# Performance work log

Measured on AMD Instinct MI355X. Metric: run time of the kernel, lower is better.

## Reference

```python
import jax, jax.numpy as jnp
import numpy as np

N = 50000   # nodes
E = 800000  # edges (avg degree 16)
D = 128     # in_feats == out_feats


def setup_inputs() -> dict:
    key = jax.random.key(0)
    k1, k2, k3, k4 = jax.random.split(key, 4)
    h = jax.random.normal(k1, (N, D), dtype=jnp.float32)
    src = jax.random.randint(k2, (E,), 0, N, dtype=jnp.int32)
    dst = jax.random.randint(k3, (E,), 0, N, dtype=jnp.int32)
    snorm_n = jnp.ones((N, 1), dtype=jnp.float32)  # sqrt(1/N) replicated; identity-scaled here
    # NodeApply linear: Linear(2*D, D) with bias
    W = jax.random.normal(k4, (D, 2 * D), dtype=jnp.float32) / np.sqrt(2 * D).astype(np.float32)
    b = jnp.zeros((D,), dtype=jnp.float32)
    return {"h": h, "snorm_n": snorm_n, "W": W, "b": b, "src": src, "dst": dst}


def reference(h, snorm_n, W, b, src, dst):
    # dropout p=0.0 -> identity
    h_in = h
    # gather neighbor messages and segment-mean aggregate (MeanAggregator)
    ones = jnp.ones((src.shape[0],), dtype=h.dtype)
    deg = jax.ops.segment_sum(ones, dst, num_segments=N)            # [N]
    msg_sum = jax.ops.segment_sum(h[src], dst, num_segments=N)     # [N, D]
    c = msg_sum / jnp.maximum(deg, 1.0)[:, None]                   # zero-degree nodes -> c = 0
    # NodeApply: concat -> linear -> L2 normalize -> relu
    bundle = jnp.concatenate([h, c], axis=1) @ W.T + b             # [N, D]
    nrm = jnp.sqrt(jnp.sum(bundle * bundle, axis=1, keepdims=True))
    bundle = bundle / jnp.maximum(nrm, 1e-12)                      # F.normalize(p=2, dim=1)
    out = jax.nn.relu(bundle)
    # graph norm
    out = out * snorm_n
    # residual (in_feats == out_feats)
    return h_in + out
```

## Files before the change

kernel.cpp:

```cpp
#include <hip/hip_runtime.h>
#include <hip/hip_bf16.h>

#define TPB 256
#define CHUNK_LOG 13
#define CHUNK (1 << CHUNK_LOG)
#define HSTRIDE 12544

typedef __attribute__((ext_vector_type(8))) short bf16x8;
typedef __attribute__((ext_vector_type(4))) float f32x4;

__device__ inline unsigned short f2bf(float f) {
    unsigned u = __float_as_uint(f);
    unsigned r = u + 0x7fffu + ((u >> 16) & 1u);
    return (unsigned short)(r >> 16);
}
__device__ inline float bf2f(unsigned short s) {
    return __uint_as_float(((unsigned)s) << 16);
}
__device__ inline float lo16(unsigned u) { return __uint_as_float(u << 16); }
__device__ inline float hi16(unsigned u) { return __uint_as_float(u & 0xffff0000u); }

__global__ void k_conv(const float* __restrict__ h, const float* __restrict__ W,
                       unsigned short* __restrict__ h_hi,
                       unsigned short* __restrict__ Wb, int N) {
    int t = blockIdx.x * TPB + threadIdx.x;
    int nh4 = N * 32;
    if (t < nh4) {
        float4 v = ((const float4*)h)[t];
        ushort4 hi;
        hi.x = f2bf(v.x); hi.y = f2bf(v.y);
        hi.z = f2bf(v.z); hi.w = f2bf(v.w);
        ((ushort4*)h_hi)[t] = hi;
    } else if (t - nh4 < 8192) {
        int w4 = t - nh4;
        float4 v = ((const float4*)W)[w4];
        ushort4 hi;
        hi.x = f2bf(v.x); hi.y = f2bf(v.y);
        hi.z = f2bf(v.z); hi.w = f2bf(v.w);
        ((ushort4*)Wb)[w4] = hi;
    }
}

__global__ void k_hist(const int* __restrict__ dst,
                       unsigned* __restrict__ hist32, unsigned char* __restrict__ lrank,
                       int E) {
    __shared__ unsigned lhist[HSTRIDE];
    int b = blockIdx.x;
    for (int i = threadIdx.x; i < HSTRIDE; i += TPB) lhist[i] = 0;
    __syncthreads();
    int e0 = b << CHUNK_LOG;
    int e1 = min(e0 + CHUNK, E);
    for (int e = e0 + (int)threadIdx.x; e < e1; e += TPB) {
        int d = dst[e];
        unsigned sh = (d & 3) * 8;
        unsigned old = atomicAdd(&lhist[d >> 2], 1u << sh);
        lrank[e] = (unsigned char)((old >> sh) & 0xffu);
    }
    __syncthreads();
    for (int i = threadIdx.x; i < HSTRIDE; i += TPB)
        hist32[(size_t)b * HSTRIDE + i] = lhist[i];
}

__global__ void k_colscan(const unsigned* __restrict__ hist32,
                          unsigned short* __restrict__ cbase, int* __restrict__ deg,
                          int* __restrict__ bsum, int N, int NBH) {
    extern __shared__ unsigned tile[];
    __shared__ int sdata[4];
    int tileBase = blockIdx.x * 64;
    int total = NBH * 64;
    for (int i = threadIdx.x; i < total; i += TPB) {
        int b = i >> 6, c = i & 63;
        tile[i] = hist32[(size_t)b * HSTRIDE + tileBase + c];
    }
    __syncthreads();
    int t = threadIdx.x;
    int n = blockIdx.x * TPB + t;
    unsigned sh = (t & 3) * 8;
    int wcol = t >> 2;
    int run = 0;
    for (int b = 0; b < NBH; ++b) {
        int c = (int)((tile[b * 64 + wcol] >> sh) & 0xffu);
        if (n < N) cbase[(size_t)b * N + n] = (unsigned short)run;
        run += c;
    }
    if (n < N) deg[n] = run; else run = 0;
    int s = run;
    for (int o = 32; o; o >>= 1) s += __shfl_xor(s, o);
    int lane = t & 63, w = t >> 6;
    if (lane == 0) sdata[w] = s;
    __syncthreads();
    if (t == 0) bsum[blockIdx.x] = sdata[0] + sdata[1] + sdata[2] + sdata[3];
}

__global__ void k_offs2(const int* __restrict__ deg, const int* __restrict__ bsum,
                        int* __restrict__ offs, int N, int E) {
    __shared__ int sb[TPB];
    __shared__ int wsum[4];
    int NB = gridDim.x;
    int t = threadIdx.x;
    int lane = t & 63, w = t >> 6;
    int v = (t < NB) ? bsum[t] : 0;
    int x = v;
    for (int o = 1; o < 64; o <<= 1) { int y = __shfl_up(x, o); if (lane >= o) x += y; }
    if (lane == 63) wsum[w] = x;
    __syncthreads();
    int add = 0;
    for (int k = 0; k < w; ++k) add += wsum[k];
    sb[t] = add + x - v;
    __syncthreads();
    int base = sb[blockIdx.x];
    int i = blockIdx.x * TPB + t;
    int dv = (i < N) ? deg[i] : 0;
    int y2 = dv;
    for (int o = 1; o < 64; o <<= 1) { int z = __shfl_up(y2, o); if (lane >= o) y2 += z; }
    __syncthreads();
    if (lane == 63) wsum[w] = y2;
    __syncthreads();
    int add2 = 0;
    for (int k = 0; k < w; ++k) add2 += wsum[k];
    int ex = base + add2 + y2 - dv;
    if (i < N) offs[i] = ex;
    if (i == N - 1) offs[N] = E;
}

__global__ void k_scatter(const int* __restrict__ src, const int* __restrict__ dst,
                          const unsigned char* __restrict__ lrank,
                          const unsigned short* __restrict__ cbase,
                          const int* __restrict__ offs,
                          unsigned short* __restrict__ esrc, int N, int E, int nchunk) {
    int slice = blockIdx.x & 7;
    int chunk = blockIdx.x >> 3;
    int lo = (int)((long long)N * slice >> 3);
    int hi = (int)((long long)N * (slice + 1) >> 3);
    for (int e = chunk * TPB + threadIdx.x; e < E; e += nchunk * TPB) {
        int d = dst[e];
        if (d >= lo && d < hi) {
            int b = e >> CHUNK_LOG;
            int pos = offs[d] + (int)cbase[(size_t)b * N + d] + (int)lrank[e];
            esrc[pos] = (unsigned short)src[e];
        }
    }
}

__launch_bounds__(TPB)
__global__ void k_apply(const unsigned short* __restrict__ h_hi,
                        const int* __restrict__ offs,
                        const unsigned short* __restrict__ esrc,
                        const unsigned short* __restrict__ Wb,
                        const float* __restrict__ bia,
                        const float* __restrict__ snorm,
                        float* __restrict__ out, int N) {
    __shared__ unsigned short c_lds[4][32][128];
    int tid = threadIdx.x;
    int lane = tid & 63;
    int l15 = lane & 15, l4 = lane >> 4;
    int wave = tid >> 6;
    int r0 = blockIdx.x * 128 + wave * 32;

    int q = l4;
    for (int i4 = 0; i4 < 32; i4 += 4) {
        int i = i4 + q;
        int n = r0 + i; if (n > N - 1) n = N - 1;
        int beg = offs[n], end = offs[n + 1];
        float a[8] = {0.f, 0.f, 0.f, 0.f, 0.f, 0.f, 0.f, 0.f};
        int e = beg;
        for (; e + 3 < end; e += 4) {
            int s0 = esrc[e], s1 = esrc[e + 1], s2 = esrc[e + 2], s3 = esrc[e + 3];
            uint4 u0 = ((const uint4*)(h_hi + (size_t)s0 * 128))[l15];
            uint4 u1 = ((const uint4*)(h_hi + (size_t)s1 * 128))[l15];
            uint4 u2 = ((const uint4*)(h_hi + (size_t)s2 * 128))[l15];
            uint4 u3 = ((const uint4*)(h_hi + (size_t)s3 * 128))[l15];
            a[0] += lo16(u0.x) + lo16(u1.x) + lo16(u2.x) + lo16(u3.x);
            a[1] += hi16(u0.x) + hi16(u1.x) + hi16(u2.x) + hi16(u3.x);
            a[2] += lo16(u0.y) + lo16(u1.y) + lo16(u2.y) + lo16(u3.y);
            a[3] += hi16(u0.y) + hi16(u1.y) + hi16(u2.y) + hi16(u3.y);
            a[4] += lo16(u0.z) + lo16(u1.z) + lo16(u2.z) + lo16(u3.z);
            a[5] += hi16(u0.z) + hi16(u1.z) + hi16(u2.z) + hi16(u3.z);
            a[6] += lo16(u0.w) + lo16(u1.w) + lo16(u2.w) + lo16(u3.w);
            a[7] += hi16(u0.w) + hi16(u1.w) + hi16(u2.w) + hi16(u3.w);
        }
        for (; e < end; ++e) {
            uint4 u0 = ((const uint4*)(h_hi + (size_t)esrc[e] * 128))[l15];
            a[0] += lo16(u0.x); a[1] += hi16(u0.x);
            a[2] += lo16(u0.y); a[3] += hi16(u0.y);
            a[4] += lo16(u0.z); a[5] += hi16(u0.z);
            a[6] += lo16(u0.w); a[7] += hi16(u0.w);
        }
        float inv = 1.0f / fmaxf((float)(end - beg), 1.0f);
        uint4 pk;
        pk.x = ((unsigned)f2bf(a[1] * inv) << 16) | (unsigned)f2bf(a[0] * inv);
        pk.y = ((unsigned)f2bf(a[3] * inv) << 16) | (unsigned)f2bf(a[2] * inv);
        pk.z = ((unsigned)f2bf(a[5] * inv) << 16) | (unsigned)f2bf(a[4] * inv);
        pk.w = ((unsigned)f2bf(a[7] * inv) << 16) | (unsigned)f2bf(a[6] * inv);
        int gs = l15 ^ (i & 7);
        ((uint4*)&c_lds[wave][i][0])[gs] = pk;
    }
    __syncthreads();

    f32x4 acc[2][8] = {};
    #pragma unroll
    for (int kc = 0; kc < 8; ++kc) {
        bf16x8 Bf[8];
        #pragma unroll
        for (int n = 0; n < 8; ++n) {
            Bf[n] = *(const bf16x8*)((const char*)Wb +
                     ((size_t)(n * 16 + l15) * 512 + (size_t)kc * 64 + (size_t)l4 * 16));
        }
        #pragma unroll
        for (int rf = 0; rf < 2; ++rf) {
            int i = rf * 16 + l15;
            bf16x8 av;
            if (kc < 4) {
                int row = r0 + i; if (row > N - 1) row = N - 1;
                av = *(const bf16x8*)((const char*)h_hi +
                      ((size_t)row * 256 + (size_t)kc * 64 + (size_t)l4 * 16));
            } else {
                int gi = (kc - 4) * 4 + l4;
                int gsw = gi ^ (i & 7);
                av = *(const bf16x8*)((const char*)&c_lds[wave][i][0] + gsw * 16);
            }
            #pragma unroll
            for (int n = 0; n < 8; ++n)
                acc[rf][n] = __builtin_amdgcn_mfma_f32_16x16x32_bf16(av, Bf[n], acc[rf][n], 0, 0, 0);
        }
    }

    float bn[8];
    #pragma unroll
    for (int n = 0; n < 8; ++n) bn[n] = bia[n * 16 + l15];

    #pragma unroll
    for (int rf = 0; rf < 2; ++rf) {
        float sq[4] = {0.f, 0.f, 0.f, 0.f};
        #pragma unroll
        for (int n = 0; n < 8; ++n) {
            #pragma unroll
            for (int g = 0; g < 4; ++g) {
                acc[rf][n][g] += bn[n];
                sq[g] += acc[rf][n][g] * acc[rf][n][g];
            }
        }
        #pragma unroll
        for (int g = 0; g < 4; ++g) {
            sq[g] += __shfl_xor(sq[g], 1);
            sq[g] += __shfl_xor(sq[g], 2);
            sq[g] += __shfl_xor(sq[g], 4);
            sq[g] += __shfl_xor(sq[g], 8);
        }
        #pragma unroll
        for (int g = 0; g < 4; ++g) {
            int row = r0 + rf * 16 + l4 * 4 + g;
            if (row < N) {
                float invn = 1.0f / fmaxf(sqrtf(sq[g]), 1e-12f);
                float sn = snorm[row];
                #pragma unroll
                for (int n = 0; n < 8; ++n) {
                    int col = n * 16 + l15;
                    float res = bf2f(h_hi[(size_t)row * 128 + col]);
                    out[(size_t)row * 128 + col] =
                        fmaxf(acc[rf][n][g] * invn, 0.f) * sn + res;
                }
            }
        }
    }
}

extern "C" void kernel_launch(void* const* d_in, const int* in_sizes, int n_in,
                              void* d_out, int out_size, void* d_ws, size_t ws_size,
                              hipStream_t stream) {
    const float* h     = (const float*)d_in[0];
    const float* snorm = (const float*)d_in[1];
    const float* W     = (const float*)d_in[2];
    const float* b     = (const float*)d_in[3];
    const int*   src   = (const int*)d_in[4];
    const int*   dst   = (const int*)d_in[5];
    int N = in_sizes[1];
    int E = in_sizes[4];
    float* out = (float*)d_out;

    char* ws = (char*)d_ws;
    size_t off = 0;
    auto alloc = [&](size_t bytes) {
        void* ptr = ws + off;
        off = (off + bytes + 255) & ~(size_t)255;
        return ptr;
    };
    int NB  = (N + TPB - 1) / TPB;
    int NBH = (E + CHUNK - 1) >> CHUNK_LOG;
    int* deg    = (int*)alloc((size_t)N * 4);
    int* offs   = (int*)alloc((size_t)(N + 1) * 4);
    int* bsum   = (int*)alloc((size_t)NB * 4);
    unsigned* hist32       = (unsigned*)alloc((size_t)NBH * HSTRIDE * 4);
    unsigned short* cbase  = (unsigned short*)alloc((size_t)NBH * N * 2);
    unsigned char*  lrank  = (unsigned char*)alloc((size_t)E);
    unsigned short* esrc   = (unsigned short*)alloc((size_t)E * 2);
    unsigned short* h_hi   = (unsigned short*)alloc((size_t)N * 128 * 2);
    unsigned short* Wb     = (unsigned short*)alloc((size_t)128 * 256 * 2);

    int conv_blocks = (N * 32 + 8192 + TPB - 1) / TPB;
    k_conv<<<conv_blocks, TPB, 0, stream>>>(h, W, h_hi, Wb, N);

    k_hist<<<NBH, TPB, 0, stream>>>(dst, hist32, lrank, E);

    size_t tile_bytes = (size_t)NBH * 64 * 4;
    k_colscan<<<NB, TPB, tile_bytes, stream>>>(hist32, cbase, deg, bsum, N, NBH);
    k_offs2<<<NB, TPB, 0, stream>>>(deg, bsum, offs, N, E);

    int nchunk = 512;
    k_scatter<<<8 * nchunk, TPB, 0, stream>>>(src, dst, lrank, cbase, offs, esrc, N, E, nchunk);

    int nblk = (N + 127) / 128;
    k_apply<<<nblk, TPB, 0, stream>>>(h_hi, offs, esrc, Wb, b, snorm, out, N);
}
```

Baseline: 123.4 us.

## Split neighbor aggregation into a separate wave-per-node kernel

The mean aggregation moves out of the MFMA apply kernel into a new kernel where each 64-lane wave handles one node and each lane gathers 4 bytes per neighbor row. The bf16 result goes to a global buffer that reuses the hist32 workspace, and k_apply reads it in place of LDS. The goal is to fix the low parallelism and load imbalance of doing the gather inside the 128-row GEMM blocks. In exchange it adds a kernel launch and a global round trip of the aggregated features (about 12.8 MB).

New measurement: 114.1 us. -7.5%, faster.

```diff
diff --git a/kernel.cpp b/kernel.cpp
--- a/kernel.cpp
+++ b/kernel.cpp
@@ -17,8 +17,6 @@
 __device__ inline float bf2f(unsigned short s) {
     return __uint_as_float(((unsigned)s) << 16);
 }
-__device__ inline float lo16(unsigned u) { return __uint_as_float(u << 16); }
-__device__ inline float hi16(unsigned u) { return __uint_as_float(u & 0xffff0000u); }
 
 __global__ void k_conv(const float* __restrict__ h, const float* __restrict__ W,
                        unsigned short* __restrict__ h_hi,
@@ -142,62 +140,52 @@
     }
 }
 
+__global__ void k_agg(const unsigned short* __restrict__ h_hi, const int* __restrict__ offs,
+                      const unsigned short* __restrict__ esrc,
+                      unsigned* __restrict__ c, int N) {
+    int wid = (blockIdx.x * TPB + threadIdx.x) >> 6;
+    int lane = threadIdx.x & 63;
+    if (wid >= N) return;
+    int beg = offs[wid], end = offs[wid + 1];
+    const unsigned* h2 = (const unsigned*)h_hi;
+    float ax0 = 0.f, ay0 = 0.f, ax1 = 0.f, ay1 = 0.f;
+    int e = beg;
+    for (; e + 3 < end; e += 4) {
+        int s0 = esrc[e], s1 = esrc[e + 1], s2 = esrc[e + 2], s3 = esrc[e + 3];
+        unsigned u0 = h2[(size_t)s0 * 64 + lane];
+        unsigned u1 = h2[(size_t)s1 * 64 + lane];
+        unsigned u2 = h2[(size_t)s2 * 64 + lane];
+        unsigned u3 = h2[(size_t)s3 * 64 + lane];
+        ax0 += __uint_as_float(u0 << 16) + __uint_as_float(u1 << 16);
+        ay0 += __uint_as_float(u0 & 0xffff0000u) + __uint_as_float(u1 & 0xffff0000u);
+        ax1 += __uint_as_float(u2 << 16) + __uint_as_float(u3 << 16);
+        ay1 += __uint_as_float(u2 & 0xffff0000u) + __uint_as_float(u3 & 0xffff0000u);
+    }
+    for (; e < end; ++e) {
+        unsigned u0 = h2[(size_t)esrc[e] * 64 + lane];
+        ax0 += __uint_as_float(u0 << 16);
+        ay0 += __uint_as_float(u0 & 0xffff0000u);
+    }
+    float ax = ax0 + ax1, ay = ay0 + ay1;
+    float inv = 1.0f / fmaxf((float)(end - beg), 1.0f);
+    unsigned pk = ((unsigned)f2bf(ay * inv) << 16) | (unsigned)f2bf(ax * inv);
+    c[(size_t)wid * 64 + lane] = pk;
+}
+
 __launch_bounds__(TPB)
 __global__ void k_apply(const unsigned short* __restrict__ h_hi,
-                        const int* __restrict__ offs,
-                        const unsigned short* __restrict__ esrc,
+                        const unsigned short* __restrict__ c,
                         const unsigned short* __restrict__ Wb,
                         const float* __restrict__ bia,
                         const float* __restrict__ snorm,
                         float* __restrict__ out, int N) {
-    __shared__ unsigned short c_lds[4][32][128];
-    int tid = threadIdx.x;
-    int lane = tid & 63;
+    int lane = threadIdx.x & 63;
     int l15 = lane & 15, l4 = lane >> 4;
-    int wave = tid >> 6;
+    int wave = threadIdx.x >> 6;
     int r0 = blockIdx.x * 128 + wave * 32;
 
-    int q = l4;
-    for (int i4 = 0; i4 < 32; i4 += 4) {
-        int i = i4 + q;
-        int n = r0 + i; if (n > N - 1) n = N - 1;
-        int beg = offs[n], end = offs[n + 1];
-        float a[8] = {0.f, 0.f, 0.f, 0.f, 0.f, 0.f, 0.f, 0.f};
-        int e = beg;
-        for (; e + 3 < end; e += 4) {
-            int s0 = esrc[e], s1 = esrc[e + 1], s2 = esrc[e + 2], s3 = esrc[e + 3];
-            uint4 u0 = ((const uint4*)(h_hi + (size_t)s0 * 128))[l15];
-            uint4 u1 = ((const uint4*)(h_hi + (size_t)s1 * 128))[l15];
-            uint4 u2 = ((const uint4*)(h_hi + (size_t)s2 * 128))[l15];
-            uint4 u3 = ((const uint4*)(h_hi + (size_t)s3 * 128))[l15];
-            a[0] += lo16(u0.x) + lo16(u1.x) + lo16(u2.x) + lo16(u3.x);
-            a[1] += hi16(u0.x) + hi16(u1.x) + hi16(u2.x) + hi16(u3.x);
-            a[2] += lo16(u0.y) + lo16(u1.y) + lo16(u2.y) + lo16(u3.y);
-            a[3] += hi16(u0.y) + hi16(u1.y) + hi16(u2.y) + hi16(u3.y);
-            a[4] += lo16(u0.z) + lo16(u1.z) + lo16(u2.z) + lo16(u3.z);
-            a[5] += hi16(u0.z) + hi16(u1.z) + hi16(u2.z) + hi16(u3.z);
-            a[6] += lo16(u0.w) + lo16(u1.w) + lo16(u2.w) + lo16(u3.w);
-            a[7] += hi16(u0.w) + hi16(u1.w) + hi16(u2.w) + hi16(u3.w);
-        }
-        for (; e < end; ++e) {
-            uint4 u0 = ((const uint4*)(h_hi + (size_t)esrc[e] * 128))[l15];
-            a[0] += lo16(u0.x); a[1] += hi16(u0.x);
-            a[2] += lo16(u0.y); a[3] += hi16(u0.y);
-            a[4] += lo16(u0.z); a[5] += hi16(u0.z);
-            a[6] += lo16(u0.w); a[7] += hi16(u0.w);
-        }
-        float inv = 1.0f / fmaxf((float)(end - beg), 1.0f);
-        uint4 pk;
-        pk.x = ((unsigned)f2bf(a[1] * inv) << 16) | (unsigned)f2bf(a[0] * inv);
-        pk.y = ((unsigned)f2bf(a[3] * inv) << 16) | (unsigned)f2bf(a[2] * inv);
-        pk.z = ((unsigned)f2bf(a[5] * inv) << 16) | (unsigned)f2bf(a[4] * inv);
-        pk.w = ((unsigned)f2bf(a[7] * inv) << 16) | (unsigned)f2bf(a[6] * inv);
-        int gs = l15 ^ (i & 7);
-        ((uint4*)&c_lds[wave][i][0])[gs] = pk;
-    }
-    __syncthreads();
-
     f32x4 acc[2][8] = {};
+
     #pragma unroll
     for (int kc = 0; kc < 8; ++kc) {
         bf16x8 Bf[8];
@@ -208,16 +196,15 @@
         }
         #pragma unroll
         for (int rf = 0; rf < 2; ++rf) {
-            int i = rf * 16 + l15;
+            int row = r0 + rf * 16 + l15;
+            if (row > N - 1) row = N - 1;
             bf16x8 av;
             if (kc < 4) {
-                int row = r0 + i; if (row > N - 1) row = N - 1;
                 av = *(const bf16x8*)((const char*)h_hi +
                       ((size_t)row * 256 + (size_t)kc * 64 + (size_t)l4 * 16));
             } else {
-                int gi = (kc - 4) * 4 + l4;
-                int gsw = gi ^ (i & 7);
-                av = *(const bf16x8*)((const char*)&c_lds[wave][i][0] + gsw * 16);
+                av = *(const bf16x8*)((const char*)c +
+                      ((size_t)row * 256 + (size_t)(kc - 4) * 64 + (size_t)l4 * 16));
             }
             #pragma unroll
             for (int n = 0; n < 8; ++n)
@@ -296,6 +283,7 @@
     unsigned short* esrc   = (unsigned short*)alloc((size_t)E * 2);
     unsigned short* h_hi   = (unsigned short*)alloc((size_t)N * 128 * 2);
     unsigned short* Wb     = (unsigned short*)alloc((size_t)128 * 256 * 2);
+    unsigned* c = hist32;
 
     int conv_blocks = (N * 32 + 8192 + TPB - 1) / TPB;
     k_conv<<<conv_blocks, TPB, 0, stream>>>(h, W, h_hi, Wb, N);
@@ -309,6 +297,8 @@
     int nchunk = 512;
     k_scatter<<<8 * nchunk, TPB, 0, stream>>>(src, dst, lrank, cbase, offs, esrc, N, E, nchunk);
 
+    k_agg<<<((size_t)N * 64 + TPB - 1) / TPB, TPB, 0, stream>>>(h_hi, offs, esrc, c, N);
+
     int nblk = (N + 127) / 128;
-    k_apply<<<nblk, TPB, 0, stream>>>(h_hi, offs, esrc, Wb, b, snorm, out, N);
-}
+    k_apply<<<nblk, TPB, 0, stream>>>(h_hi, (const unsigned short*)c, Wb, b, snorm, out, N);
+}
```
